# Optimization experiments

Hardware: AMD Instinct MI355X
Metric: run time of the kernel (lower is better)

The kernel has to match this reference:

```python
import jax, jax.numpy as jnp
import numpy as np

GAMMAK = 1.0 / 256.0  # 1/(2*d) so kernel values don't underflow for unit-gaussian data


def setup_inputs() -> dict:
    key = jax.random.key(0)
    k1, k2, k3, k4, k5 = jax.random.split(key, 5)
    N, d = 8192, 128
    X = jax.random.normal(k1, (N, d), dtype=jnp.float32)
    y = jax.random.normal(k2, (N - 1, d), dtype=jnp.float32)
    y_next = jax.random.normal(k3, (N - 1, d), dtype=jnp.float32)
    # reset_transform initializes R=eye, t=0; perturb slightly for nontrivial math
    R = jnp.eye(d, dtype=jnp.float32) + 0.01 * jax.random.normal(k4, (d, d), dtype=jnp.float32)
    t = 0.01 * jax.random.normal(k5, (d, 1), dtype=jnp.float32)
    return {"X": X, "y": y, "y_next": y_next, "R": R, "t": t}


def reference(X, y, y_next, R, t):
    # _transform_pts: (R @ y.T + t).T == y @ R.T + t.squeeze()
    yt = y @ R.T + t[:, 0]            # (N-1, d)
    Xb = X[:-1]                        # (N-1, d) kernel base points
    # pairwise_sqeuclidean(Xb, yt), clamped at 0
    sq = jnp.clip(
        jnp.sum(Xb * Xb, axis=1)[:, None]
        + jnp.sum(yt * yt, axis=1)[None, :]
        - 2.0 * (Xb @ yt.T),
        0.0, None,
    )                                  # (N-1, N-1)
    G = jnp.exp(-GAMMAK * sq)
    # diag(1/rowsum) @ G  ==  G / rowsum[:, None]  (avoids explicit NxN diagonal)
    y_pred = (G / jnp.sum(G, axis=1, keepdims=True)) @ X[1:]  # (N-1, d)
    return y_pred
```

## Files before the change

### kernel.cpp

```cpp
#include <hip/hip_runtime.h>


#define LOG2E 1.44269504088896340736f
#define KNEG (-(1.0f/256.0f)*LOG2E)
#define KA2C (2.0f*(1.0f/256.0f)*LOG2E)

typedef __attribute__((ext_vector_type(4)))  float f32x4;
typedef __attribute__((ext_vector_type(16))) float f32x16;
typedef __attribute__((ext_vector_type(8)))  short bf16x8;
typedef __attribute__((ext_vector_type(4)))  short bf16x4;

#if __has_builtin(__builtin_amdgcn_mfma_f32_32x32x8bf16_1k)
#define PV_DIRECT 1
#else
#define PV_DIRECT 0
#endif

__device__ __forceinline__ unsigned short f2bf(float f) {
  unsigned u = __builtin_bit_cast(unsigned, f);
  u = (u + 0x7fffu + ((u >> 16) & 1u)) >> 16;
  return (unsigned short)u;
}
__device__ __forceinline__ unsigned pk2bf(float a, float b) {
  return (unsigned)f2bf(a) | ((unsigned)f2bf(b) << 16);
}
__device__ __forceinline__ bf16x8 pack8(float4 p0, float4 p1) {
  uint4 u;
  u.x = pk2bf(p0.x, p0.y); u.y = pk2bf(p0.z, p0.w);
  u.z = pk2bf(p1.x, p1.y); u.w = pk2bf(p1.z, p1.w);
  return __builtin_bit_cast(bf16x8, u);
}
__device__ __forceinline__ float fast_exp2(float x) {
#if __has_builtin(__builtin_amdgcn_exp2f)
  return __builtin_amdgcn_exp2f(x);
#else
  return exp2f(x);
#endif
}
__device__ __forceinline__ void gl2lds16(const void* g, void* l) {
  __builtin_amdgcn_global_load_lds((const __attribute__((address_space(1))) unsigned int*)g,
                                   (__attribute__((address_space(3))) unsigned int*)l, 16, 0, 0);
}
__device__ __forceinline__ void gl2lds4(const void* g, void* l) {
  __builtin_amdgcn_global_load_lds((const __attribute__((address_space(1))) unsigned int*)g,
                                   (__attribute__((address_space(3))) unsigned int*)l, 4, 0, 0);
}
__device__ __forceinline__ f32x16 mfma_32x32x16(bf16x8 a, bf16x8 b, f32x16 c) {
  return __builtin_amdgcn_mfma_f32_32x32x16_bf16(a, b, c, 0, 0, 0);
}
#if PV_DIRECT
__device__ __forceinline__ f32x16 mfma_32x32x8(bf16x4 a, bf16x4 b, f32x16 c) {
  return __builtin_amdgcn_mfma_f32_32x32x8bf16_1k(a, b, c, 0, 0, 0);
}
#endif

__global__ __launch_bounds__(256) void k_prep(const float* __restrict__ y,
                                              const float* __restrict__ R,
                                              const float* __restrict__ t,
                                              const float* __restrict__ X,
                                              unsigned short* __restrict__ ytp,
                                              float* __restrict__ ynp,
                                              unsigned short* __restrict__ x1tp,
                                              float* __restrict__ xnp) {
  __shared__ union {
    unsigned short ytt[128 * 132];
    struct { float xt[65 * 132]; float ps[64][4]; } xb;
  } sm;
  const int tid = threadIdx.x;

  if (blockIdx.x < 64) {
    const int wv = tid >> 6, ln = tid & 63;
    const int l = ln & 31, h = ln >> 5;
    const int B = blockIdx.x;
    const int rw = B * 128 + wv * 32;

    bf16x8 af[8];
    {
      int row = rw + l; if (row > 8190) row = 8190;
      const float* yr = y + (size_t)row * 128;
#pragma unroll
      for (int kc = 0; kc < 8; ++kc) {
        float4 p0 = *(const float4*)(yr + kc*16 + 8*h);
        float4 p1 = *(const float4*)(yr + kc*16 + 8*h + 4);
        af[kc] = pack8(p0, p1);
      }
    }
    f32x16 acc[4];
#pragma unroll
    for (int cc=0; cc<4; ++cc)
#pragma unroll
      for (int i=0;i<16;++i) acc[cc][i] = 0.f;
#pragma unroll
    for (int cc=0; cc<4; ++cc) {
      const float* Rr = R + (size_t)(cc*32 + l) * 128;
#pragma unroll
      for (int kc=0; kc<8; ++kc) {
        float4 p0 = *(const float4*)(Rr + kc*16 + 8*h);
        float4 p1 = *(const float4*)(Rr + kc*16 + 8*h + 4);
        acc[cc] = mfma_32x32x16(af[kc], pack8(p0, p1), acc[cc]);
      }
    }
    float tv0 = t[l], tv1 = t[32+l], tv2 = t[64+l], tv3 = t[96+l];
    float v0[16], v1[16], v2[16], v3[16], ssq[16];
#pragma unroll
    for (int r=0;r<16;++r) {
      v0[r]=acc[0][r]+tv0; v1[r]=acc[1][r]+tv1; v2[r]=acc[2][r]+tv2; v3[r]=acc[3][r]+tv3;
      ssq[r] = v0[r]*v0[r] + v1[r]*v1[r] + v2[r]*v2[r] + v3[r]*v3[r];
    }
#pragma unroll
    for (int off=1; off<32; off<<=1)
#pragma unroll
      for (int r=0;r<16;++r) ssq[r] += __shfl_xor(ssq[r], off, 64);
    if (l < 16) {
      int r = l;
      int row = rw + (r&3) + 8*(r>>2) + 4*h;
      float val = KNEG * ssq[r];
      if (row >= 8191) val = -1e30f;
      ynp[row] = val;
    }
#pragma unroll
    for (int r=0;r<16;++r) {
      int rloc = wv*32 + (r&3) + 8*(r>>2) + 4*h;
      sm.ytt[rloc*132 +   0 + l] = f2bf(v0[r]);
      sm.ytt[rloc*132 +  32 + l] = f2bf(v1[r]);
      sm.ytt[rloc*132 +  64 + l] = f2bf(v2[r]);
      sm.ytt[rloc*132 +  96 + l] = f2bf(v3[r]);
    }
    __syncthreads();
    const int Tt = B*2 + (wv>>1);
    const int jcw = wv & 1;
#pragma unroll
    for (int kc=0;kc<8;++kc) {
      const unsigned short* s = &sm.ytt[(wv*32 + l)*132 + kc*16 + 8*h];
      uint2 a = *(const uint2*)(s);
      uint2 b = *(const uint2*)(s + 4);
      uint4 o; o.x=a.x; o.y=a.y; o.z=b.x; o.w=b.y;
      *(uint4*)(ytp + (size_t)Tt*8192 + jcw*4096 + kc*512 + ln*8) = o;
    }
  } else {
    const int T = blockIdx.x - 64;
    const int jt = T * 64;
    {
      int rr = tid >> 2, q4 = tid & 3;
      int row = jt + rr; if (row > 8191) row = 8191;
      const float* src = X + (size_t)row*128 + q4*32;
      float* dst = &sm.xb.xt[rr*132 + q4*32];
      float s = 0.f;
#pragma unroll
      for (int i=0;i<8;++i) {
        float4 p = *(const float4*)(src + i*4);
        s += p.x*p.x + p.y*p.y + p.z*p.z + p.w*p.w;
        *(float4*)(dst + i*4) = p;
      }
      sm.xb.ps[rr][q4] = s;
      if (tid < 4) {
        int row2 = jt + 64; if (row2 > 8191) row2 = 8191;
        const float* s2 = X + (size_t)row2*128 + tid*32;
        float* d2 = &sm.xb.xt[64*132 + tid*32];
#pragma unroll
        for (int i=0;i<8;++i) *(float4*)(d2 + i*4) = *(const float4*)(s2 + i*4);
      }
    }
    __syncthreads();
    if (tid < 64) xnp[jt + tid] = KNEG * (sm.xb.ps[tid][0] + sm.xb.ps[tid][1] +
                                          sm.xb.ps[tid][2] + sm.xb.ps[tid][3]);
#if PV_DIRECT
#pragma unroll
    for (int it=0; it<8; ++it) {
      int E = tid + it*256;
      int lp = E & 63, grp = E >> 6;
      int cc = grp & 3, s = (grp >> 2) & 3, jc = grp >> 4;
      int jb = jc*32 + s*8 + 4*(lp>>5);
      int c  = cc*32 + (lp & 31);
      uint2 o;
      o.x = pk2bf(sm.xb.xt[(jb+1)*132 + c], sm.xb.xt[(jb+2)*132 + c]);
      o.y = pk2bf(sm.xb.xt[(jb+3)*132 + c], sm.xb.xt[(jb+4)*132 + c]);
      *(uint2*)(x1tp + (size_t)T*8192 + E*4) = o;
    }
#else
#pragma unroll
    for (int it=0; it<4; ++it) {
      int E = tid + it*256;
      int lp = E & 63, grp = E >> 6;
      int cc = grp & 3, jc16 = grp >> 2;
      int jb = jc16*16 + 8*(lp>>5);
      int c  = cc*32 + (lp & 31);
      uint4 o;
      o.x = pk2bf(sm.xb.xt[(jb+1)*132 + c], sm.xb.xt[(jb+2)*132 + c]);
      o.y = pk2bf(sm.xb.xt[(jb+3)*132 + c], sm.xb.xt[(jb+4)*132 + c]);
      o.z = pk2bf(sm.xb.xt[(jb+5)*132 + c], sm.xb.xt[(jb+6)*132 + c]);
      o.w = pk2bf(sm.xb.xt[(jb+7)*132 + c], sm.xb.xt[(jb+8)*132 + c]);
      *(uint4*)(x1tp + (size_t)T*8192 + E*8) = o;
    }
#endif
  }
}

__global__ __launch_bounds__(256, 3) void k_main(
    const float* __restrict__ X,
    const unsigned short* __restrict__ ytp,
    const unsigned short* __restrict__ x1tp,
    const float* __restrict__ xnp,
    const float* __restrict__ ynp,
    float* __restrict__ accp,
    float* __restrict__ rsp,
    int js) {
  __shared__ unsigned short yts[8192];
  __shared__ unsigned short vts[8192];
  __shared__ float yns[64];
#if !PV_DIRECT
  __shared__ unsigned short gls[4*32*68];
#endif
  const int tid = threadIdx.x;
  const int wv = tid >> 6, ln = tid & 63;
  const int l = ln & 31, h = ln >> 5;
  const int row = blockIdx.x*128 + wv*32 + l;

  bf16x8 qf[8];
  {
    const float* xr = X + (size_t)row * 128;
#pragma unroll
    for (int kc=0;kc<8;++kc) {
      float4 p0 = *(const float4*)(xr + kc*16 + 8*h);
      float4 p1 = *(const float4*)(xr + kc*16 + 8*h + 4);
      qf[kc] = pack8(p0, p1);
    }
  }
  const float xnl = xnp[row];
  f32x16 acc[4];
#pragma unroll
  for (int cc=0;cc<4;++cc)
#pragma unroll
    for (int i=0;i<16;++i) acc[cc][i]=0.f;
  float rs = 0.f;
  const int sp = blockIdx.y;
  const int Tbeg = (sp * 128) / js;
  const int Tend = ((sp + 1) * 128) / js;
  for (int T = Tbeg; T < Tend; ++T) {
    __syncthreads();
    {
      const char* yb = (const char*)(ytp + (size_t)T*8192);
      const char* vb = (const char*)(x1tp + (size_t)T*8192);
#pragma unroll
      for (int i=0;i<4;++i) {
        int off = (wv*4 + i) * 1024;
        gl2lds16(yb + off + ln*16, (char*)yts + off);
        gl2lds16(vb + off + ln*16, (char*)vts + off);
      }
      if (wv == 0) gl2lds4(ynp + T*64 + ln, (char*)yns);
    }
    __syncthreads();
#pragma unroll
    for (int jc=0; jc<2; ++jc) {
      f32x16 sa;
#pragma unroll
      for (int i=0;i<16;++i) sa[i]=0.f;
#pragma unroll
      for (int kc=0;kc<8;++kc) {
        bf16x8 a = *(const bf16x8*)((const char*)yts + (jc*8+kc)*1024 + ln*16);
        sa = mfma_32x32x16(a, qf[kc], sa);
      }
      float gg[16];
#pragma unroll
      for (int rg=0; rg<4; ++rg) {
        f32x4 yv = *(const f32x4*)((const char*)yns + (jc*32 + rg*8 + 4*h)*4);
#pragma unroll
        for (int i=0;i<4;++i) {
          float e = fmaf(sa[rg*4+i], KA2C, xnl + yv[i]);
          e = fminf(e, 0.f);
          float g = fast_exp2(e);
          gg[rg*4+i] = g;
          rs += g;
        }
      }
#if PV_DIRECT
      bf16x4 pf[4];
#pragma unroll
      for (int s=0;s<4;++s) {
        uint2 u;
        u.x = pk2bf(gg[4*s+0], gg[4*s+1]);
        u.y = pk2bf(gg[4*s+2], gg[4*s+3]);
        pf[s] = __builtin_bit_cast(bf16x4, u);
      }
#pragma unroll
      for (int s=0;s<4;++s)
#pragma unroll
        for (int cc=0;cc<4;++cc) {
          bf16x4 a = *(const bf16x4*)((const char*)vts + ((jc*16 + s*4 + cc)*512) + ln*8);
          acc[cc] = mfma_32x32x8(a, pf[s], acc[cc]);
        }
#else
#pragma unroll
      for (int p=0;p<8;++p) {
        int j0 = jc*32 + 2*(p&1) + 8*(p>>1) + 4*h;
        *(unsigned*)&gls[(wv*32 + l)*68 + j0] = pk2bf(gg[2*p], gg[2*p+1]);
      }
      __builtin_amdgcn_wave_barrier();
#pragma unroll
      for (int jj=0; jj<2; ++jj) {
        int jc16 = jc*2 + jj;
        const unsigned short* gp = &gls[(wv*32 + l)*68 + jc16*16 + 8*h];
        uint2 g0 = *(const uint2*)(gp);
        uint2 g1 = *(const uint2*)(gp + 4);
        uint4 gv; gv.x=g0.x; gv.y=g0.y; gv.z=g1.x; gv.w=g1.y;
        bf16x8 pb = __builtin_bit_cast(bf16x8, gv);
#pragma unroll
        for (int cc=0;cc<4;++cc) {
          bf16x8 a2 = *(const bf16x8*)((const char*)vts + (jc16*4+cc)*1024 + ln*16);
          acc[cc] = mfma_32x32x16(a2, pb, acc[cc]);
        }
      }
      __builtin_amdgcn_wave_barrier();
#endif
    }
  }
  rs += __shfl_xor(rs, 32, 64);
  if (h == 0) rsp[(size_t)sp*8192 + row] = rs;
#pragma unroll
  for (int cc=0;cc<4;++cc)
#pragma unroll
    for (int r=0;r<16;++r) {
      int c = cc*32 + (r&3) + 8*(r>>2) + 4*h;
      accp[((size_t)sp*128 + c)*8192 + row] = acc[cc][r];
    }
}

__global__ __launch_bounds__(256) void k_fin(const float* __restrict__ accp,
                                             const float* __restrict__ rsp,
                                             float* __restrict__ out,
                                             int js) {
  __shared__ float tr[64*132];
  __shared__ float rinv[64];
  const int tid = threadIdx.x;
  const int r0 = blockIdx.x * 64;
  if (tid < 64) {
    float s = 0.f;
    for (int sp=0; sp<js; ++sp) s += rsp[(size_t)sp*8192 + r0 + tid];
    rinv[tid] = 1.f / s;
  }
  const int rq = tid & 15, cg = tid >> 4;
  float v[8][4];
#pragma unroll
  for (int cc=0;cc<8;++cc)
#pragma unroll
    for (int k=0;k<4;++k) v[cc][k]=0.f;
  for (int sp=0; sp<js; ++sp) {
    const float* base = accp + ((size_t)sp*128 + cg*8)*8192 + r0 + rq*4;
#pragma unroll
    for (int cc=0; cc<8; ++cc) {
      float4 p = *(const float4*)(base + (size_t)cc*8192);
      v[cc][0]+=p.x; v[cc][1]+=p.y; v[cc][2]+=p.z; v[cc][3]+=p.w;
    }
  }
  __syncthreads();
#pragma unroll
  for (int cc=0;cc<8;++cc)
#pragma unroll
    for (int k=0;k<4;++k)
      tr[(rq*4+k)*132 + cg*8+cc] = v[cc][k] * rinv[rq*4+k];
  __syncthreads();
  {
    int r = tid >> 2, q = tid & 3;
    int grow = r0 + r;
    if (grow < 8191) {
      float* dst = out + (size_t)grow*128 + q*32;
      const float* s2 = &tr[r*132 + q*32];
#pragma unroll
      for (int i=0;i<8;++i) *(float4*)(dst + i*4) = *(const float4*)(s2 + i*4);
    }
  }
}

extern "C" void kernel_launch(void* const* d_in, const int* in_sizes, int n_in,
                              void* d_out, int out_size, void* d_ws, size_t ws_size,
                              hipStream_t stream) {
  const float* X = (const float*)d_in[0];
  const float* y = (const float*)d_in[1];
  const float* R = (const float*)d_in[3];
  const float* t = (const float*)d_in[4];
  float* out = (float*)d_out;
  char* ws = (char*)d_ws;

  unsigned short* ytp  = (unsigned short*)(ws);
  unsigned short* x1tp = (unsigned short*)(ws + (size_t)8192*128*2);
  float* ynp = (float*)(ws + (size_t)4*1024*1024);
  float* xnp = (float*)(ws + (size_t)4*1024*1024 + 32*1024);
  float* rsp = (float*)(ws + (size_t)4*1024*1024 + 64*1024);
  size_t accoff = (size_t)4*1024*1024 + 64*1024 + 512*1024;
  float* accp = (float*)(ws + accoff);

  int js = 12;
  while (js > 1 && accoff + (size_t)js*128*8192*4 > ws_size) js >>= 1;

  k_prep<<<dim3(192), dim3(256), 0, stream>>>(y, R, t, X, ytp, ynp, x1tp, xnp);
  k_main<<<dim3(64, js), dim3(256), 0, stream>>>(X, ytp, x1tp, xnp, ynp, accp, rsp, js);
  k_fin<<<dim3(128), dim3(256), 0, stream>>>(accp, rsp, out, js);
}
```

Baseline: 144.7 us.

## Fold norm terms and scaling into augmented bf16 MFMA K-dimension

Pre-scales transformed y by the exponent constant and appends a ninth K-chunk holding the y-norm split into hi/lo bf16, paired with a ones column on the query side. The exponent therefore comes straight out of the MFMA, which removes the per-element fma, the min clamp and the separate y-norm load. The x-norm term is dropped entirely because it cancels in the row normalisation. The y and value tiles are merged into one contiguous staged buffer per tile, loaded with a single global-to-LDS pass, and the PV_DIRECT path is removed. Risks are bf16 precision loss in the folded norm and exponent, and overflow of exp2 without the clamp, since the row exponent is no longer shifted by the x-norm.

```diff
diff --git a/kernel.cpp b/kernel.cpp
--- a/kernel.cpp
+++ b/kernel.cpp
@@ -1,4 +1,5 @@
 #include <hip/hip_runtime.h>
+#include <hip/hip_bf16.h>
 
 
 #define LOG2E 1.44269504088896340736f
@@ -8,13 +9,6 @@
 typedef __attribute__((ext_vector_type(4)))  float f32x4;
 typedef __attribute__((ext_vector_type(16))) float f32x16;
 typedef __attribute__((ext_vector_type(8)))  short bf16x8;
-typedef __attribute__((ext_vector_type(4)))  short bf16x4;
-
-#if __has_builtin(__builtin_amdgcn_mfma_f32_32x32x8bf16_1k)
-#define PV_DIRECT 1
-#else
-#define PV_DIRECT 0
-#endif
 
 __device__ __forceinline__ unsigned short f2bf(float f) {
   unsigned u = __builtin_bit_cast(unsigned, f);
@@ -22,7 +16,10 @@
   return (unsigned short)u;
 }
 __device__ __forceinline__ unsigned pk2bf(float a, float b) {
-  return (unsigned)f2bf(a) | ((unsigned)f2bf(b) << 16);
+  __hip_bfloat162 h = __float22bfloat162_rn(float2{a, b});
+  unsigned u;
+  __builtin_memcpy(&u, &h, 4);
+  return u;
 }
 __device__ __forceinline__ bf16x8 pack8(float4 p0, float4 p1) {
   uint4 u;
@@ -41,30 +38,21 @@
   __builtin_amdgcn_global_load_lds((const __attribute__((address_space(1))) unsigned int*)g,
                                    (__attribute__((address_space(3))) unsigned int*)l, 16, 0, 0);
 }
-__device__ __forceinline__ void gl2lds4(const void* g, void* l) {
-  __builtin_amdgcn_global_load_lds((const __attribute__((address_space(1))) unsigned int*)g,
-                                   (__attribute__((address_space(3))) unsigned int*)l, 4, 0, 0);
-}
 __device__ __forceinline__ f32x16 mfma_32x32x16(bf16x8 a, bf16x8 b, f32x16 c) {
   return __builtin_amdgcn_mfma_f32_32x32x16_bf16(a, b, c, 0, 0, 0);
 }
-#if PV_DIRECT
-__device__ __forceinline__ f32x16 mfma_32x32x8(bf16x4 a, bf16x4 b, f32x16 c) {
-  return __builtin_amdgcn_mfma_f32_32x32x8bf16_1k(a, b, c, 0, 0, 0);
-}
-#endif
+
+#define T_STRIDE 34816
+#define V_OFF    18432
 
 __global__ __launch_bounds__(256) void k_prep(const float* __restrict__ y,
                                               const float* __restrict__ R,
                                               const float* __restrict__ t,
                                               const float* __restrict__ X,
-                                              unsigned short* __restrict__ ytp,
-                                              float* __restrict__ ynp,
-                                              unsigned short* __restrict__ x1tp,
-                                              float* __restrict__ xnp) {
+                                              unsigned short* __restrict__ ctp) {
   __shared__ union {
-    unsigned short ytt[128 * 132];
-    struct { float xt[65 * 132]; float ps[64][4]; } xb;
+    struct { unsigned short ytt[128 * 132]; float ynl[128]; } yb;
+    float xt[65 * 132];
   } sm;
   const int tid = threadIdx.x;
 
@@ -113,29 +101,38 @@
       for (int r=0;r<16;++r) ssq[r] += __shfl_xor(ssq[r], off, 64);
     if (l < 16) {
       int r = l;
-      int row = rw + (r&3) + 8*(r>>2) + 4*h;
-      float val = KNEG * ssq[r];
-      if (row >= 8191) val = -1e30f;
-      ynp[row] = val;
+      int rloc = wv*32 + (r&3) + 8*(r>>2) + 4*h;
+      int grow = rw + (r&3) + 8*(r>>2) + 4*h;
+      sm.yb.ynl[rloc] = (grow >= 8191) ? -1.0e4f : KNEG * ssq[r];
     }
 #pragma unroll
     for (int r=0;r<16;++r) {
       int rloc = wv*32 + (r&3) + 8*(r>>2) + 4*h;
-      sm.ytt[rloc*132 +   0 + l] = f2bf(v0[r]);
-      sm.ytt[rloc*132 +  32 + l] = f2bf(v1[r]);
-      sm.ytt[rloc*132 +  64 + l] = f2bf(v2[r]);
-      sm.ytt[rloc*132 +  96 + l] = f2bf(v3[r]);
+      sm.yb.ytt[rloc*132 +   0 + l] = f2bf(KA2C * v0[r]);
+      sm.yb.ytt[rloc*132 +  32 + l] = f2bf(KA2C * v1[r]);
+      sm.yb.ytt[rloc*132 +  64 + l] = f2bf(KA2C * v2[r]);
+      sm.yb.ytt[rloc*132 +  96 + l] = f2bf(KA2C * v3[r]);
     }
     __syncthreads();
     const int Tt = B*2 + (wv>>1);
     const int jcw = wv & 1;
+    char* base = (char*)ctp + (size_t)Tt*T_STRIDE;
 #pragma unroll
     for (int kc=0;kc<8;++kc) {
-      const unsigned short* s = &sm.ytt[(wv*32 + l)*132 + kc*16 + 8*h];
+      const unsigned short* s = &sm.yb.ytt[(wv*32 + l)*132 + kc*16 + 8*h];
       uint2 a = *(const uint2*)(s);
       uint2 b = *(const uint2*)(s + 4);
       uint4 o; o.x=a.x; o.y=a.y; o.z=b.x; o.w=b.y;
-      *(uint4*)(ytp + (size_t)Tt*8192 + jcw*4096 + kc*512 + ln*8) = o;
+      *(uint4*)(base + (jcw*9 + kc)*1024 + ln*16) = o;
+    }
+    {
+      float yn = sm.yb.ynl[wv*32 + l];
+      unsigned short hi = f2bf(yn);
+      float hif = __builtin_bit_cast(float, (unsigned)hi << 16);
+      unsigned short lo = f2bf(yn - hif);
+      uint4 o; o.x = (h == 0) ? ((unsigned)hi | ((unsigned)lo << 16)) : 0u;
+      o.y = 0u; o.z = 0u; o.w = 0u;
+      *(uint4*)(base + (jcw*9 + 8)*1024 + ln*16) = o;
     }
   } else {
     const int T = blockIdx.x - 64;
@@ -144,40 +141,19 @@
       int rr = tid >> 2, q4 = tid & 3;
       int row = jt + rr; if (row > 8191) row = 8191;
       const float* src = X + (size_t)row*128 + q4*32;
-      float* dst = &sm.xb.xt[rr*132 + q4*32];
-      float s = 0.f;
-#pragma unroll
-      for (int i=0;i<8;++i) {
-        float4 p = *(const float4*)(src + i*4);
-        s += p.x*p.x + p.y*p.y + p.z*p.z + p.w*p.w;
-        *(float4*)(dst + i*4) = p;
-      }
-      sm.xb.ps[rr][q4] = s;
+      float* dst = &sm.xt[rr*132 + q4*32];
+#pragma unroll
+      for (int i=0;i<8;++i) *(float4*)(dst + i*4) = *(const float4*)(src + i*4);
       if (tid < 4) {
         int row2 = jt + 64; if (row2 > 8191) row2 = 8191;
         const float* s2 = X + (size_t)row2*128 + tid*32;
-        float* d2 = &sm.xb.xt[64*132 + tid*32];
+        float* d2 = &sm.xt[64*132 + tid*32];
 #pragma unroll
         for (int i=0;i<8;++i) *(float4*)(d2 + i*4) = *(const float4*)(s2 + i*4);
       }
     }
     __syncthreads();
-    if (tid < 64) xnp[jt + tid] = KNEG * (sm.xb.ps[tid][0] + sm.xb.ps[tid][1] +
-                                          sm.xb.ps[tid][2] + sm.xb.ps[tid][3]);
-#if PV_DIRECT
-#pragma unroll
-    for (int it=0; it<8; ++it) {
-      int E = tid + it*256;
-      int lp = E & 63, grp = E >> 6;
-      int cc = grp & 3, s = (grp >> 2) & 3, jc = grp >> 4;
-      int jb = jc*32 + s*8 + 4*(lp>>5);
-      int c  = cc*32 + (lp & 31);
-      uint2 o;
-      o.x = pk2bf(sm.xb.xt[(jb+1)*132 + c], sm.xb.xt[(jb+2)*132 + c]);
-      o.y = pk2bf(sm.xb.xt[(jb+3)*132 + c], sm.xb.xt[(jb+4)*132 + c]);
-      *(uint2*)(x1tp + (size_t)T*8192 + E*4) = o;
-    }
-#else
+    char* base = (char*)ctp + (size_t)T*T_STRIDE + V_OFF;
 #pragma unroll
     for (int it=0; it<4; ++it) {
       int E = tid + it*256;
@@ -186,37 +162,29 @@
       int jb = jc16*16 + 8*(lp>>5);
       int c  = cc*32 + (lp & 31);
       uint4 o;
-      o.x = pk2bf(sm.xb.xt[(jb+1)*132 + c], sm.xb.xt[(jb+2)*132 + c]);
-      o.y = pk2bf(sm.xb.xt[(jb+3)*132 + c], sm.xb.xt[(jb+4)*132 + c]);
-      o.z = pk2bf(sm.xb.xt[(jb+5)*132 + c], sm.xb.xt[(jb+6)*132 + c]);
-      o.w = pk2bf(sm.xb.xt[(jb+7)*132 + c], sm.xb.xt[(jb+8)*132 + c]);
-      *(uint4*)(x1tp + (size_t)T*8192 + E*8) = o;
-    }
-#endif
+      o.x = pk2bf(sm.xt[(jb+1)*132 + c], sm.xt[(jb+2)*132 + c]);
+      o.y = pk2bf(sm.xt[(jb+3)*132 + c], sm.xt[(jb+4)*132 + c]);
+      o.z = pk2bf(sm.xt[(jb+5)*132 + c], sm.xt[(jb+6)*132 + c]);
+      o.w = pk2bf(sm.xt[(jb+7)*132 + c], sm.xt[(jb+8)*132 + c]);
+      *(uint4*)(base + E*16) = o;
+    }
   }
 }
 
 __global__ __launch_bounds__(256, 3) void k_main(
     const float* __restrict__ X,
-    const unsigned short* __restrict__ ytp,
-    const unsigned short* __restrict__ x1tp,
-    const float* __restrict__ xnp,
-    const float* __restrict__ ynp,
+    const unsigned short* __restrict__ ctp,
     float* __restrict__ accp,
     float* __restrict__ rsp,
     int js) {
-  __shared__ unsigned short yts[8192];
-  __shared__ unsigned short vts[8192];
-  __shared__ float yns[64];
-#if !PV_DIRECT
+  __shared__ unsigned short stg[T_STRIDE/2];
   __shared__ unsigned short gls[4*32*68];
-#endif
   const int tid = threadIdx.x;
   const int wv = tid >> 6, ln = tid & 63;
   const int l = ln & 31, h = ln >> 5;
   const int row = blockIdx.x*128 + wv*32 + l;
 
-  bf16x8 qf[8];
+  bf16x8 qf[9];
   {
     const float* xr = X + (size_t)row * 128;
 #pragma unroll
@@ -225,8 +193,9 @@
       float4 p1 = *(const float4*)(xr + kc*16 + 8*h + 4);
       qf[kc] = pack8(p0, p1);
     }
-  }
-  const float xnl = xnp[row];
+    uint4 o; o.x = (h == 0) ? 0x3F803F80u : 0u; o.y = 0u; o.z = 0u; o.w = 0u;
+    qf[8] = __builtin_bit_cast(bf16x8, o);
+  }
   f32x16 acc[4];
 #pragma unroll
   for (int cc=0;cc<4;++cc)
@@ -239,15 +208,12 @@
   for (int T = Tbeg; T < Tend; ++T) {
     __syncthreads();
     {
-      const char* yb = (const char*)(ytp + (size_t)T*8192);
-      const char* vb = (const char*)(x1tp + (size_t)T*8192);
-#pragma unroll
-      for (int i=0;i<4;++i) {
-        int off = (wv*4 + i) * 1024;
-        gl2lds16(yb + off + ln*16, (char*)yts + off);
-        gl2lds16(vb + off + ln*16, (char*)vts + off);
-      }
-      if (wv == 0) gl2lds4(ynp + T*64 + ln, (char*)yns);
+      const char* cb = (const char*)ctp + (size_t)T*T_STRIDE;
+#pragma unroll
+      for (int i=0;i<9;++i) {
+        int c = wv + 4*i;
+        if (c < 34) gl2lds16(cb + c*1024 + ln*16, (char*)stg + c*1024);
+      }
     }
     __syncthreads();
 #pragma unroll
@@ -256,62 +222,37 @@
 #pragma unroll
       for (int i=0;i<16;++i) sa[i]=0.f;
 #pragma unroll
-      for (int kc=0;kc<8;++kc) {
-        bf16x8 a = *(const bf16x8*)((const char*)yts + (jc*8+kc)*1024 + ln*16);
+      for (int kc=0;kc<9;++kc) {
+        bf16x8 a = *(const bf16x8*)((const char*)stg + (jc*9+kc)*1024 + ln*16);
         sa = mfma_32x32x16(a, qf[kc], sa);
       }
-      float gg[16];
 #pragma unroll
       for (int rg=0; rg<4; ++rg) {
-        f32x4 yv = *(const f32x4*)((const char*)yns + (jc*32 + rg*8 + 4*h)*4);
-#pragma unroll
-        for (int i=0;i<4;++i) {
-          float e = fmaf(sa[rg*4+i], KA2C, xnl + yv[i]);
-          e = fminf(e, 0.f);
-          float g = fast_exp2(e);
-          gg[rg*4+i] = g;
-          rs += g;
-        }
-      }
-#if PV_DIRECT
-      bf16x4 pf[4];
-#pragma unroll
-      for (int s=0;s<4;++s) {
-        uint2 u;
-        u.x = pk2bf(gg[4*s+0], gg[4*s+1]);
-        u.y = pk2bf(gg[4*s+2], gg[4*s+3]);
-        pf[s] = __builtin_bit_cast(bf16x4, u);
-      }
-#pragma unroll
-      for (int s=0;s<4;++s)
-#pragma unroll
-        for (int cc=0;cc<4;++cc) {
-          bf16x4 a = *(const bf16x4*)((const char*)vts + ((jc*16 + s*4 + cc)*512) + ln*8);
-          acc[cc] = mfma_32x32x8(a, pf[s], acc[cc]);
-        }
-#else
-#pragma unroll
-      for (int p=0;p<8;++p) {
-        int j0 = jc*32 + 2*(p&1) + 8*(p>>1) + 4*h;
-        *(unsigned*)&gls[(wv*32 + l)*68 + j0] = pk2bf(gg[2*p], gg[2*p+1]);
+        float g0 = fast_exp2(sa[rg*4+0]);
+        float g1 = fast_exp2(sa[rg*4+1]);
+        float g2 = fast_exp2(sa[rg*4+2]);
+        float g3 = fast_exp2(sa[rg*4+3]);
+        rs += (g0+g1) + (g2+g3);
+        uint2 w; w.x = pk2bf(g0, g1); w.y = pk2bf(g2, g3);
+        int j0 = jc*32 + 8*rg + 4*h;
+        *(uint2*)&gls[(wv*32+l)*68 + j0] = w;
       }
       __builtin_amdgcn_wave_barrier();
 #pragma unroll
       for (int jj=0; jj<2; ++jj) {
         int jc16 = jc*2 + jj;
-        const unsigned short* gp = &gls[(wv*32 + l)*68 + jc16*16 + 8*h];
+        const unsigned short* gp = &gls[(wv*32+l)*68 + jc16*16 + 8*h];
         uint2 g0 = *(const uint2*)(gp);
         uint2 g1 = *(const uint2*)(gp + 4);
         uint4 gv; gv.x=g0.x; gv.y=g0.y; gv.z=g1.x; gv.w=g1.y;
         bf16x8 pb = __builtin_bit_cast(bf16x8, gv);
 #pragma unroll
         for (int cc=0;cc<4;++cc) {
-          bf16x8 a2 = *(const bf16x8*)((const char*)vts + (jc16*4+cc)*1024 + ln*16);
+          bf16x8 a2 = *(const bf16x8*)((const char*)stg + V_OFF + (jc16*4+cc)*1024 + ln*16);
           acc[cc] = mfma_32x32x16(a2, pb, acc[cc]);
         }
       }
       __builtin_amdgcn_wave_barrier();
-#endif
     }
   }
   rs += __shfl_xor(rs, 32, 64);
@@ -381,18 +322,16 @@
   float* out = (float*)d_out;
   char* ws = (char*)d_ws;
 
-  unsigned short* ytp  = (unsigned short*)(ws);
-  unsigned short* x1tp = (unsigned short*)(ws + (size_t)8192*128*2);
-  float* ynp = (float*)(ws + (size_t)4*1024*1024);
-  float* xnp = (float*)(ws + (size_t)4*1024*1024 + 32*1024);
-  float* rsp = (float*)(ws + (size_t)4*1024*1024 + 64*1024);
-  size_t accoff = (size_t)4*1024*1024 + 64*1024 + 512*1024;
+  unsigned short* ctp = (unsigned short*)ws;
+  size_t rspoff = (size_t)128 * T_STRIDE;
+  float* rsp  = (float*)(ws + rspoff);
+  size_t accoff = rspoff + 512*1024;
   float* accp = (float*)(ws + accoff);
 
   int js = 12;
   while (js > 1 && accoff + (size_t)js*128*8192*4 > ws_size) js >>= 1;
 
-  k_prep<<<dim3(192), dim3(256), 0, stream>>>(y, R, t, X, ytp, ynp, x1tp, xnp);
-  k_main<<<dim3(64, js), dim3(256), 0, stream>>>(X, ytp, x1tp, xnp, ynp, accp, rsp, js);
+  k_prep<<<dim3(192), dim3(256), 0, stream>>>(y, R, t, X, ctp);
+  k_main<<<dim3(64, js), dim3(256), 0, stream>>>(X, ctp, accp, rsp, js);
   k_fin<<<dim3(128), dim3(256), 0, stream>>>(accp, rsp, out, js);
 }
```

Measured after the change: 140.3 us. -3.1%, faster.
